# Performance work log

Measured on AMD Instinct MI355X. Metric: run time of the kernel, lower is better.

The kernel has to match this reference:

```python
import jax, jax.numpy as jnp
import numpy as np

B, N, F, H = 64, 1024, 128, 256  # graphs, nodes per graph, nfeat, nhid


def setup_inputs() -> dict:
    key = jax.random.key(0)
    ks = jax.random.split(key, 8)
    s_in = 1.0 / np.sqrt(F)
    s_h = 1.0 / np.sqrt(H)
    return {
        "embs": jax.random.normal(ks[0], (B, N, F), jnp.float32),
        "adjmat": jax.random.uniform(ks[1], (B, N, N), jnp.float32) / N,  # row-scaled dense adjacency
        "W0": jax.random.normal(ks[2], (F, H), jnp.float32) * s_in,
        "b0": jnp.zeros((H,), jnp.float32),
        "W1": jax.random.normal(ks[3], (H, H), jnp.float32) * s_h,
        "b1": jnp.zeros((H,), jnp.float32),
        "W2": jax.random.normal(ks[4], (H, H), jnp.float32) * s_h,
        "b2": jnp.zeros((H,), jnp.float32),
        "Wl": jax.random.normal(ks[5], (H, F), jnp.float32) * s_h,
        "bl": jnp.zeros((F,), jnp.float32),
    }


def reference(embs, adjmat, W0, b0, W1, b1, W2, b2, Wl, bl):
    # Batched form of the per-graph loop: every adj is N x N, so the
    # x[:adj.shape[0]] slice is identity and all graphs fuse into one GEMM.
    hid = embs  # [B, N, F]
    for W, b in ((W0, b0), (W1, b1), (W2, b2)):
        # GraphConvolution: adj @ (x @ W) + b, then relu
        hid = jax.nn.relu(jnp.einsum('bnm,bmh->bnh', adjmat, hid @ W) + b)
    out = hid @ Wl + bl          # [B, N, F] linear_hid
    return out[:, 0, :]          # hid[0] per graph -> [B, F]
```

## Files before the change

### kernel.cpp

```cpp
#include <hip/hip_runtime.h>
#include <stdint.h>

typedef __bf16 bf16;
typedef __bf16 bf16x8 __attribute__((ext_vector_type(8)));
typedef float f32x4 __attribute__((ext_vector_type(4)));

enum { EPI_STORE = 0, EPI_BIAS_RELU = 1, EPI_VRED = 2 };

__device__ __forceinline__ void gload16(const bf16* g, bf16* l) {
  __builtin_amdgcn_global_load_lds(
      (const __attribute__((address_space(1))) unsigned int*)g,
      (__attribute__((address_space(3))) unsigned int*)l, 16, 0, 0);
}

template<bool A_F32, int EPI, bool WRITE_A16>
__global__ __launch_bounds__(256, 2)
void gemm_bt(const void* __restrict__ Ap, const bf16* __restrict__ Btp,
             const float* __restrict__ bias, bf16* __restrict__ C,
             float* __restrict__ vpart, const float* __restrict__ adjp,
             bf16* __restrict__ A16,
             int K, int ldA, int ldBt, int ldC,
             long sA, long sBt, long sC)
{
  constexpr int BM = 128, BN = 256, BK = 32;
  __shared__ __align__(16) bf16 As[3][BM * BK];
  __shared__ __align__(16) bf16 Bs[3][BN * BK];
  __shared__ float a0s[BM];
  __shared__ float vsum[BN];

  const int tid  = threadIdx.x;
  const int lane = tid & 63;
  const int wid  = tid >> 6;
  const int wm   = wid >> 1;
  const int wn   = wid & 1;
  const int l15  = lane & 15;
  const int quad = lane >> 4;

  const int nb = blockIdx.x, mb = blockIdx.y, g = blockIdx.z;

  const long aoff = (long)g * sA + (long)mb * BM * ldA;
  const long boff = (long)g * sBt + (long)nb * BN * ldBt;

  if constexpr (EPI == EPI_VRED) {
    if (tid < BM) a0s[tid] = adjp[(long)g * sA + mb * BM + tid];
    vsum[tid] = 0.f;
  }

  const int r   = tid >> 2;
  const int c4  = tid & 3;
  const int sw  = (r >> 1) & 3;
  const int kcs = (c4 ^ sw) << 3;
  const int kcp = c4 << 3;
  const int csw = (quad ^ ((l15 >> 1) & 3)) << 3;

  const bf16* Bg0 = Btp + boff;

  auto issueB = [&](int s, int buf) {
    const bf16* Bg = Bg0 + s * BK;
    #pragma unroll
    for (int p = 0; p < 4; ++p)
      gload16(Bg + (long)(p * 64 + r) * ldBt + kcs, &Bs[buf][p * 2048 + tid * 8]);
  };
  auto issueAg = [&](int s, int buf) {
    const bf16* Ag = (const bf16*)Ap + aoff + s * BK;
    #pragma unroll
    for (int p = 0; p < 2; ++p)
      gload16(Ag + (long)(p * 64 + r) * ldA + kcs, &As[buf][p * 2048 + tid * 8]);
  };
  auto issueAf = [&](int s, float4 (&pf)[4]) {
    const float* Ag = (const float*)Ap + aoff + s * BK;
    #pragma unroll
    for (int p = 0; p < 2; ++p) {
      const float4* src = (const float4*)(Ag + (long)(p * 64 + r) * ldA + kcp);
      pf[p * 2 + 0] = src[0];
      pf[p * 2 + 1] = src[1];
    }
  };
  auto commitAf = [&](int s, float4 (&pf)[4], int buf) {
    #pragma unroll
    for (int p = 0; p < 2; ++p) {
      float4 v0 = pf[p * 2 + 0], v1 = pf[p * 2 + 1];
      bf16x8 w;
      w[0]=(bf16)v0.x; w[1]=(bf16)v0.y; w[2]=(bf16)v0.z; w[3]=(bf16)v0.w;
      w[4]=(bf16)v1.x; w[5]=(bf16)v1.y; w[6]=(bf16)v1.z; w[7]=(bf16)v1.w;
      *(bf16x8*)&As[buf][p * 2048 + r * 32 + kcs] = w;
      if constexpr (WRITE_A16)
        *(bf16x8*)&A16[aoff + (long)(p * 64 + r) * ldA + s * BK + kcp] = w;
    }
  };

  f32x4 acc[4][8] = {};
  const int n = K / BK;

  if constexpr (!A_F32) {
    issueAg(0, 0); issueB(0, 0);
    if (n > 1) { issueAg(1, 1); issueB(1, 1); }
    for (int s = 0; s < n; ++s) {
      const int b = s % 3;
      if (s + 2 < n) { issueAg(s + 2, (s + 2) % 3); issueB(s + 2, (s + 2) % 3); }
      if (s + 2 < n)      asm volatile("s_waitcnt vmcnt(12)" ::: "memory");
      else if (s + 1 < n) asm volatile("s_waitcnt vmcnt(6)"  ::: "memory");
      else                asm volatile("s_waitcnt vmcnt(0)"  ::: "memory");
      __builtin_amdgcn_s_barrier();

      bf16x8 af[4], bfr[8];
      #pragma unroll
      for (int i = 0; i < 4; ++i)
        af[i] = *(const bf16x8*)&As[b][(wm * 64 + i * 16 + l15) * 32 + csw];
      #pragma unroll
      for (int j = 0; j < 8; ++j)
        bfr[j] = *(const bf16x8*)&Bs[b][(wn * 128 + j * 16 + l15) * 32 + csw];
      asm volatile("s_waitcnt lgkmcnt(0)" ::: "memory");
      __builtin_amdgcn_s_barrier();

      #pragma unroll
      for (int i = 0; i < 4; ++i)
        #pragma unroll
        for (int j = 0; j < 8; ++j)
          acc[i][j] = __builtin_amdgcn_mfma_f32_16x16x32_bf16(af[i], bfr[j], acc[i][j], 0, 0, 0);
    }
  } else {
    float4 pfa[4], pfb[4];
    issueAf(0, pfa); issueB(0, 0);
    issueAf(1, pfb); issueB(1, 1);
    commitAf(0, pfa, 0);
    asm volatile("s_waitcnt lgkmcnt(0)" ::: "memory");
    __builtin_amdgcn_s_barrier();

    auto bodyF = [&](int s, float4 (&pfI)[4], float4 (&pfC)[4]) {
      const int b = s % 3;
      if (s + 2 < n) { issueAf(s + 2, pfI); issueB(s + 2, (s + 2) % 3); }
      if (s + 2 < n)      asm volatile("s_waitcnt vmcnt(16)" ::: "memory");
      else if (s + 1 < n) asm volatile("s_waitcnt vmcnt(8)"  ::: "memory");
      else                asm volatile("s_waitcnt vmcnt(0)"  ::: "memory");
      __builtin_amdgcn_s_barrier();

      bf16x8 af[4], bfr[8];
      #pragma unroll
      for (int i = 0; i < 4; ++i)
        af[i] = *(const bf16x8*)&As[b][(wm * 64 + i * 16 + l15) * 32 + csw];
      #pragma unroll
      for (int j = 0; j < 8; ++j)
        bfr[j] = *(const bf16x8*)&Bs[b][(wn * 128 + j * 16 + l15) * 32 + csw];
      if (s + 1 < n) commitAf(s + 1, pfC, (s + 1) % 3);
      asm volatile("s_waitcnt lgkmcnt(0)" ::: "memory");
      __builtin_amdgcn_s_barrier();

      #pragma unroll
      for (int i = 0; i < 4; ++i)
        #pragma unroll
        for (int j = 0; j < 8; ++j)
          acc[i][j] = __builtin_amdgcn_mfma_f32_16x16x32_bf16(af[i], bfr[j], acc[i][j], 0, 0, 0);
    };
    for (int s = 0; s < n; s += 2) { bodyF(s, pfa, pfb); bodyF(s + 1, pfb, pfa); }
  }

  if constexpr (EPI == EPI_STORE || EPI == EPI_BIAS_RELU) {
    bf16* Cg = C + (long)g * sC;
    #pragma unroll
    for (int i = 0; i < 4; ++i) {
      const int row0 = mb * BM + wm * 64 + i * 16 + quad * 4;
      #pragma unroll
      for (int j = 0; j < 8; ++j) {
        const int col = nb * BN + wn * 128 + j * 16 + l15;
        float bv = 0.f;
        if constexpr (EPI == EPI_BIAS_RELU) bv = bias[col];
        #pragma unroll
        for (int rr = 0; rr < 4; ++rr) {
          float v = acc[i][j][rr];
          if constexpr (EPI == EPI_BIAS_RELU) v = fmaxf(v + bv, 0.f);
          Cg[(long)(row0 + rr) * ldC + col] = (bf16)v;
        }
      }
    }
  } else {
    __syncthreads();
    #pragma unroll
    for (int j = 0; j < 8; ++j) {
      const int col = wn * 128 + j * 16 + l15;
      const float bv = bias[col];
      float p = 0.f;
      #pragma unroll
      for (int i = 0; i < 4; ++i) {
        const int lr = wm * 64 + i * 16 + quad * 4;
        #pragma unroll
        for (int rr = 0; rr < 4; ++rr)
          p += fmaxf(acc[i][j][rr] + bv, 0.f) * a0s[lr + rr];
      }
      atomicAdd(&vsum[col], p);
    }
    __syncthreads();
    vpart[((long)g * 8 + mb) * 256 + tid] = vsum[tid];
  }
}

__global__ void cvt1(const float* __restrict__ src, bf16* __restrict__ dst, long n8)
{
  const long stride = (long)gridDim.x * blockDim.x;
  for (long i = (long)blockIdx.x * blockDim.x + threadIdx.x; i < n8; i += stride) {
    const float4* s = (const float4*)(src + i * 8);
    float4 v0 = s[0], v1 = s[1];
    bf16x8 w;
    w[0]=(bf16)v0.x; w[1]=(bf16)v0.y; w[2]=(bf16)v0.z; w[3]=(bf16)v0.w;
    w[4]=(bf16)v1.x; w[5]=(bf16)v1.y; w[6]=(bf16)v1.z; w[7]=(bf16)v1.w;
    *(bf16x8*)(dst + i * 8) = w;
  }
}

__global__ void prep_w(const float* __restrict__ W0, const float* __restrict__ W1,
                       bf16* __restrict__ W0t, bf16* __restrict__ W1t)
{
  const int idx = blockIdx.x * 256 + threadIdx.x;
  if (idx < 256 * 128) {
    const int h = idx >> 7, k = idx & 127;
    W0t[idx] = (bf16)W0[k * 256 + h];
  }
  const int h = idx >> 8, k = idx & 255;
  W1t[idx] = (bf16)W1[k * 256 + h];
}

__global__ void finish_k(const float* __restrict__ vpart, const float* __restrict__ W2,
                         const float* __restrict__ b2, const float* __restrict__ Wl,
                         const float* __restrict__ bl, float* __restrict__ out)
{
  const int b = blockIdx.x, t = threadIdx.x;
  __shared__ float v[256], h3[256];
  float s = 0.f;
  #pragma unroll
  for (int mb = 0; mb < 8; ++mb) s += vpart[((long)b * 8 + mb) * 256 + t];
  v[t] = s;
  __syncthreads();
  float z = b2[t];
  for (int k = 0; k < 256; ++k) z += v[k] * W2[k * 256 + t];
  h3[t] = fmaxf(z, 0.f);
  __syncthreads();
  if (t < 128) {
    float o = bl[t];
    for (int h = 0; h < 256; ++h) o += h3[h] * Wl[h * 128 + t];
    out[(long)b * 128 + t] = o;
  }
}

extern "C" void kernel_launch(void* const* d_in, const int* in_sizes, int n_in,
                              void* d_out, int out_size, void* d_ws, size_t ws_size,
                              hipStream_t stream) {
  const float* embs = (const float*)d_in[0];
  const float* adj  = (const float*)d_in[1];
  const float* W0   = (const float*)d_in[2];
  const float* b0   = (const float*)d_in[3];
  const float* W1   = (const float*)d_in[4];
  const float* b1   = (const float*)d_in[5];
  const float* W2   = (const float*)d_in[6];
  const float* b2   = (const float*)d_in[7];
  const float* Wl   = (const float*)d_in[8];
  const float* bl   = (const float*)d_in[9];
  float* out = (float*)d_out;

  char* ws = (char*)d_ws;
  bf16*  Zt     = (bf16*)(ws);
  bf16*  Hb     = (bf16*)(ws + 33554432);
  bf16*  W0t    = (bf16*)(ws + 67108864);
  bf16*  W1t    = (bf16*)(ws + 67174400);
  float* vpart  = (float*)(ws + 67305472);
  bf16*  embs16 = (bf16*)(ws + 67829760);
  bf16*  adj16  = (bf16*)(ws + 134217728);

  prep_w<<<256, 256, 0, stream>>>(W0, W1, W0t, W1t);
  cvt1<<<2048, 256, 0, stream>>>(embs, embs16, 64L * 1024 * 128 / 8);

  gemm_bt<false, EPI_STORE, false><<<dim3(4, 2, 64), 256, 0, stream>>>(
      W0t, embs16, nullptr, Zt, nullptr, nullptr, nullptr,
      128, 128, 128, 1024, 0L, 131072L, 262144L);

  gemm_bt<true, EPI_BIAS_RELU, true><<<dim3(1, 8, 64), 256, 0, stream>>>(
      adj, Zt, b0, Hb, nullptr, nullptr, adj16,
      1024, 1024, 1024, 256, 1048576L, 262144L, 262144L);

  gemm_bt<false, EPI_STORE, false><<<dim3(4, 2, 64), 256, 0, stream>>>(
      W1t, Hb, nullptr, Zt, nullptr, nullptr, nullptr,
      256, 256, 256, 1024, 0L, 262144L, 262144L);

  gemm_bt<false, EPI_VRED, false><<<dim3(1, 8, 64), 256, 0, stream>>>(
      adj16, Zt, b1, nullptr, vpart, adj, nullptr,
      1024, 1024, 1024, 256, 1048576L, 262144L, 0L);

  finish_k<<<64, 256, 0, stream>>>(vpart, W2, b2, Wl, bl, out);
}
```

Measured before the change: 601.7 us.

## Drop bf16 adjacency copy, stagger K order, stage epilogue through LDS

Removes writing a bf16 copy of the adjacency during the first propagation GEMM; the second propagation now rereads fp32 adjacency with nontemporal loads and converts in-kernel. Each block starts its K loop at a rotated offset, which spreads concurrent blocks across different memory regions. The store epilogue writes the tile to a per-wave LDS slab and then issues 16-byte coalesced global stores instead of scattered 2-byte stores. In exchange, the second adj GEMM reads twice the bytes of adjacency, and the K-rotation relies on n being a power of two.

```diff
diff --git a/kernel.cpp b/kernel.cpp
--- a/kernel.cpp
+++ b/kernel.cpp
@@ -13,18 +13,18 @@
       (__attribute__((address_space(3))) unsigned int*)l, 16, 0, 0);
 }
 
-template<bool A_F32, int EPI, bool WRITE_A16>
+template<bool A_F32, int EPI>
 __global__ __launch_bounds__(256, 2)
 void gemm_bt(const void* __restrict__ Ap, const bf16* __restrict__ Btp,
              const float* __restrict__ bias, bf16* __restrict__ C,
              float* __restrict__ vpart, const float* __restrict__ adjp,
-             bf16* __restrict__ A16,
              int K, int ldA, int ldBt, int ldC,
              long sA, long sBt, long sC)
 {
   constexpr int BM = 128, BN = 256, BK = 32;
-  __shared__ __align__(16) bf16 As[3][BM * BK];
-  __shared__ __align__(16) bf16 Bs[3][BN * BK];
+  __shared__ __align__(16) char raw[73728];
+  auto Asb = [&](int b) -> bf16* { return (bf16*)(raw + b * 8192); };
+  auto Bsb = [&](int b) -> bf16* { return (bf16*)(raw + 24576 + b * 16384); };
   __shared__ float a0s[BM];
   __shared__ float vsum[BN];
 
@@ -53,51 +53,53 @@
   const int kcp = c4 << 3;
   const int csw = (quad ^ ((l15 >> 1) & 3)) << 3;
 
+  const int n  = K / BK;
+  const int nm = n - 1;
+  const int off = (g * 11 + mb * 5 + nb * 3) & nm;
+  auto kof = [&](int s) { return ((s + off) & nm) * BK; };
+
   const bf16* Bg0 = Btp + boff;
 
-  auto issueB = [&](int s, int buf) {
-    const bf16* Bg = Bg0 + s * BK;
+  auto issueB = [&](int k0, int buf) {
+    const bf16* Bg = Bg0 + k0;
     #pragma unroll
     for (int p = 0; p < 4; ++p)
-      gload16(Bg + (long)(p * 64 + r) * ldBt + kcs, &Bs[buf][p * 2048 + tid * 8]);
-  };
-  auto issueAg = [&](int s, int buf) {
-    const bf16* Ag = (const bf16*)Ap + aoff + s * BK;
+      gload16(Bg + (long)(p * 64 + r) * ldBt + kcs, Bsb(buf) + p * 2048 + tid * 8);
+  };
+  auto issueAg = [&](int k0, int buf) {
+    const bf16* Ag = (const bf16*)Ap + aoff + k0;
     #pragma unroll
     for (int p = 0; p < 2; ++p)
-      gload16(Ag + (long)(p * 64 + r) * ldA + kcs, &As[buf][p * 2048 + tid * 8]);
-  };
-  auto issueAf = [&](int s, float4 (&pf)[4]) {
-    const float* Ag = (const float*)Ap + aoff + s * BK;
+      gload16(Ag + (long)(p * 64 + r) * ldA + kcs, Asb(buf) + p * 2048 + tid * 8);
+  };
+  auto issueAf = [&](int k0, f32x4 (&pf)[4]) {
+    const float* Ag = (const float*)Ap + aoff + k0;
     #pragma unroll
     for (int p = 0; p < 2; ++p) {
-      const float4* src = (const float4*)(Ag + (long)(p * 64 + r) * ldA + kcp);
-      pf[p * 2 + 0] = src[0];
-      pf[p * 2 + 1] = src[1];
-    }
-  };
-  auto commitAf = [&](int s, float4 (&pf)[4], int buf) {
+      const f32x4* src = (const f32x4*)(Ag + (long)(p * 64 + r) * ldA + kcp);
+      pf[p * 2 + 0] = __builtin_nontemporal_load(src);
+      pf[p * 2 + 1] = __builtin_nontemporal_load(src + 1);
+    }
+  };
+  auto commitAf = [&](f32x4 (&pf)[4], int buf) {
     #pragma unroll
     for (int p = 0; p < 2; ++p) {
-      float4 v0 = pf[p * 2 + 0], v1 = pf[p * 2 + 1];
+      f32x4 v0 = pf[p * 2 + 0], v1 = pf[p * 2 + 1];
       bf16x8 w;
-      w[0]=(bf16)v0.x; w[1]=(bf16)v0.y; w[2]=(bf16)v0.z; w[3]=(bf16)v0.w;
-      w[4]=(bf16)v1.x; w[5]=(bf16)v1.y; w[6]=(bf16)v1.z; w[7]=(bf16)v1.w;
-      *(bf16x8*)&As[buf][p * 2048 + r * 32 + kcs] = w;
-      if constexpr (WRITE_A16)
-        *(bf16x8*)&A16[aoff + (long)(p * 64 + r) * ldA + s * BK + kcp] = w;
+      w[0]=(bf16)v0[0]; w[1]=(bf16)v0[1]; w[2]=(bf16)v0[2]; w[3]=(bf16)v0[3];
+      w[4]=(bf16)v1[0]; w[5]=(bf16)v1[1]; w[6]=(bf16)v1[2]; w[7]=(bf16)v1[3];
+      *(bf16x8*)(Asb(buf) + p * 2048 + r * 32 + kcs) = w;
     }
   };
 
   f32x4 acc[4][8] = {};
-  const int n = K / BK;
 
   if constexpr (!A_F32) {
-    issueAg(0, 0); issueB(0, 0);
-    if (n > 1) { issueAg(1, 1); issueB(1, 1); }
+    issueAg(kof(0), 0); issueB(kof(0), 0);
+    if (n > 1) { issueAg(kof(1), 1); issueB(kof(1), 1); }
     for (int s = 0; s < n; ++s) {
       const int b = s % 3;
-      if (s + 2 < n) { issueAg(s + 2, (s + 2) % 3); issueB(s + 2, (s + 2) % 3); }
+      if (s + 2 < n) { issueAg(kof(s + 2), (s + 2) % 3); issueB(kof(s + 2), (s + 2) % 3); }
       if (s + 2 < n)      asm volatile("s_waitcnt vmcnt(12)" ::: "memory");
       else if (s + 1 < n) asm volatile("s_waitcnt vmcnt(6)"  ::: "memory");
       else                asm volatile("s_waitcnt vmcnt(0)"  ::: "memory");
@@ -106,10 +108,10 @@
       bf16x8 af[4], bfr[8];
       #pragma unroll
       for (int i = 0; i < 4; ++i)
-        af[i] = *(const bf16x8*)&As[b][(wm * 64 + i * 16 + l15) * 32 + csw];
+        af[i] = *(const bf16x8*)(Asb(b) + (wm * 64 + i * 16 + l15) * 32 + csw);
       #pragma unroll
       for (int j = 0; j < 8; ++j)
-        bfr[j] = *(const bf16x8*)&Bs[b][(wn * 128 + j * 16 + l15) * 32 + csw];
+        bfr[j] = *(const bf16x8*)(Bsb(b) + (wn * 128 + j * 16 + l15) * 32 + csw);
       asm volatile("s_waitcnt lgkmcnt(0)" ::: "memory");
       __builtin_amdgcn_s_barrier();
 
@@ -120,16 +122,17 @@
           acc[i][j] = __builtin_amdgcn_mfma_f32_16x16x32_bf16(af[i], bfr[j], acc[i][j], 0, 0, 0);
     }
   } else {
-    float4 pfa[4], pfb[4];
-    issueAf(0, pfa); issueB(0, 0);
-    issueAf(1, pfb); issueB(1, 1);
-    commitAf(0, pfa, 0);
+    f32x4 pfa[4], pfb[4];
+    issueAf(kof(0), pfa); issueB(kof(0), 0);
+    issueAf(kof(1), pfb); issueB(kof(1), 1);
+    commitAf(pfa, 0);
+    asm volatile("s_waitcnt vmcnt(8)" ::: "memory");
     asm volatile("s_waitcnt lgkmcnt(0)" ::: "memory");
     __builtin_amdgcn_s_barrier();
 
-    auto bodyF = [&](int s, float4 (&pfI)[4], float4 (&pfC)[4]) {
+    auto bodyF = [&](int s, f32x4 (&pfI)[4], f32x4 (&pfC)[4]) {
       const int b = s % 3;
-      if (s + 2 < n) { issueAf(s + 2, pfI); issueB(s + 2, (s + 2) % 3); }
+      if (s + 2 < n) { issueAf(kof(s + 2), pfI); issueB(kof(s + 2), (s + 2) % 3); }
       if (s + 2 < n)      asm volatile("s_waitcnt vmcnt(16)" ::: "memory");
       else if (s + 1 < n) asm volatile("s_waitcnt vmcnt(8)"  ::: "memory");
       else                asm volatile("s_waitcnt vmcnt(0)"  ::: "memory");
@@ -138,11 +141,11 @@
       bf16x8 af[4], bfr[8];
       #pragma unroll
       for (int i = 0; i < 4; ++i)
-        af[i] = *(const bf16x8*)&As[b][(wm * 64 + i * 16 + l15) * 32 + csw];
+        af[i] = *(const bf16x8*)(Asb(b) + (wm * 64 + i * 16 + l15) * 32 + csw);
       #pragma unroll
       for (int j = 0; j < 8; ++j)
-        bfr[j] = *(const bf16x8*)&Bs[b][(wn * 128 + j * 16 + l15) * 32 + csw];
-      if (s + 1 < n) commitAf(s + 1, pfC, (s + 1) % 3);
+        bfr[j] = *(const bf16x8*)(Bsb(b) + (wn * 128 + j * 16 + l15) * 32 + csw);
+      if (s + 1 < n) commitAf(pfC, (s + 1) % 3);
       asm volatile("s_waitcnt lgkmcnt(0)" ::: "memory");
       __builtin_amdgcn_s_barrier();
 
@@ -156,22 +159,28 @@
   }
 
   if constexpr (EPI == EPI_STORE || EPI == EPI_BIAS_RELU) {
-    bf16* Cg = C + (long)g * sC;
-    #pragma unroll
-    for (int i = 0; i < 4; ++i) {
-      const int row0 = mb * BM + wm * 64 + i * 16 + quad * 4;
-      #pragma unroll
-      for (int j = 0; j < 8; ++j) {
-        const int col = nb * BN + wn * 128 + j * 16 + l15;
-        float bv = 0.f;
-        if constexpr (EPI == EPI_BIAS_RELU) bv = bias[col];
+    constexpr int LDW = 140;
+    bf16* slab = (bf16*)(raw + wid * 17920);
+    #pragma unroll
+    for (int j = 0; j < 8; ++j) {
+      float bv = 0.f;
+      if constexpr (EPI == EPI_BIAS_RELU) bv = bias[nb * BN + wn * 128 + j * 16 + l15];
+      #pragma unroll
+      for (int i = 0; i < 4; ++i)
         #pragma unroll
         for (int rr = 0; rr < 4; ++rr) {
           float v = acc[i][j][rr];
           if constexpr (EPI == EPI_BIAS_RELU) v = fmaxf(v + bv, 0.f);
-          Cg[(long)(row0 + rr) * ldC + col] = (bf16)v;
+          slab[(i * 16 + quad * 4 + rr) * LDW + j * 16 + l15] = (bf16)v;
         }
-      }
+    }
+    asm volatile("s_waitcnt lgkmcnt(0)" ::: "memory");
+    bf16* Cg = C + (long)g * sC + (long)(mb * BM + wm * 64) * ldC + nb * BN + wn * 128;
+    #pragma unroll
+    for (int t = 0; t < 16; ++t) {
+      const int rowl = t * 4 + quad;
+      bf16x8 w = *(const bf16x8*)&slab[rowl * LDW + l15 * 8];
+      *(bf16x8*)&Cg[(long)rowl * ldC + l15 * 8] = w;
     }
   } else {
     __syncthreads();
@@ -198,11 +207,11 @@
 {
   const long stride = (long)gridDim.x * blockDim.x;
   for (long i = (long)blockIdx.x * blockDim.x + threadIdx.x; i < n8; i += stride) {
-    const float4* s = (const float4*)(src + i * 8);
-    float4 v0 = s[0], v1 = s[1];
+    const f32x4* s = (const f32x4*)(src + i * 8);
+    f32x4 v0 = s[0], v1 = s[1];
     bf16x8 w;
-    w[0]=(bf16)v0.x; w[1]=(bf16)v0.y; w[2]=(bf16)v0.z; w[3]=(bf16)v0.w;
-    w[4]=(bf16)v1.x; w[5]=(bf16)v1.y; w[6]=(bf16)v1.z; w[7]=(bf16)v1.w;
+    w[0]=(bf16)v0[0]; w[1]=(bf16)v0[1]; w[2]=(bf16)v0[2]; w[3]=(bf16)v0[3];
+    w[4]=(bf16)v1[0]; w[5]=(bf16)v1[1]; w[6]=(bf16)v1[2]; w[7]=(bf16)v1[3];
     *(bf16x8*)(dst + i * 8) = w;
   }
 }
@@ -263,25 +272,24 @@
   bf16*  W1t    = (bf16*)(ws + 67174400);
   float* vpart  = (float*)(ws + 67305472);
   bf16*  embs16 = (bf16*)(ws + 67829760);
-  bf16*  adj16  = (bf16*)(ws + 134217728);
 
   prep_w<<<256, 256, 0, stream>>>(W0, W1, W0t, W1t);
   cvt1<<<2048, 256, 0, stream>>>(embs, embs16, 64L * 1024 * 128 / 8);
 
-  gemm_bt<false, EPI_STORE, false><<<dim3(4, 2, 64), 256, 0, stream>>>(
-      W0t, embs16, nullptr, Zt, nullptr, nullptr, nullptr,
+  gemm_bt<false, EPI_STORE><<<dim3(4, 2, 64), 256, 0, stream>>>(
+      W0t, embs16, nullptr, Zt, nullptr, nullptr,
       128, 128, 128, 1024, 0L, 131072L, 262144L);
 
-  gemm_bt<true, EPI_BIAS_RELU, true><<<dim3(1, 8, 64), 256, 0, stream>>>(
-      adj, Zt, b0, Hb, nullptr, nullptr, adj16,
+  gemm_bt<true, EPI_BIAS_RELU><<<dim3(1, 8, 64), 256, 0, stream>>>(
+      adj, Zt, b0, Hb, nullptr, nullptr,
       1024, 1024, 1024, 256, 1048576L, 262144L, 262144L);
 
-  gemm_bt<false, EPI_STORE, false><<<dim3(4, 2, 64), 256, 0, stream>>>(
-      W1t, Hb, nullptr, Zt, nullptr, nullptr, nullptr,
+  gemm_bt<false, EPI_STORE><<<dim3(4, 2, 64), 256, 0, stream>>>(
+      W1t, Hb, nullptr, Zt, nullptr, nullptr,
       256, 256, 256, 1024, 0L, 262144L, 262144L);
 
-  gemm_bt<false, EPI_VRED, false><<<dim3(1, 8, 64), 256, 0, stream>>>(
-      adj16, Zt, b1, nullptr, vpart, adj, nullptr,
+  gemm_bt<true, EPI_VRED><<<dim3(1, 8, 64), 256, 0, stream>>>(
+      adj, Zt, b1, nullptr, vpart, adj,
       1024, 1024, 1024, 256, 1048576L, 262144L, 0L);
 
   finish_k<<<64, 256, 0, stream>>>(vpart, W2, b2, Wl, bl, out);
```

Result: faster. 550.8 us (-8.5%).
